# Performance work log

Hardware: AMD Instinct MI355X
Metric: run time of the kernel (lower is better)

The kernel has to match this reference:

```python
import jax, jax.numpy as jnp
import numpy as np

N_NODES = 50000
N_EDGES = 800000
IN_DIM = 128
HID_DIM = 128
OUT_DIM = 64


def setup_inputs() -> dict:
    key = jax.random.key(0)
    ks = jax.random.split(key, 6)
    x = jax.random.normal(ks[0], (N_NODES, IN_DIM), dtype=jnp.float32)
    edge_index = jax.random.randint(ks[1], (2, N_EDGES), 0, N_NODES, dtype=jnp.int64)
    # per-hop linear weights (torch Linear layout: [out, in], no bias)
    s = 1.0 / np.sqrt(IN_DIM)
    W0 = jax.random.uniform(ks[2], (HID_DIM, IN_DIM), jnp.float32, -s, s)
    W1 = jax.random.uniform(ks[3], (HID_DIM, IN_DIM), jnp.float32, -s, s)
    W2 = jax.random.uniform(ks[4], (HID_DIM, IN_DIM), jnp.float32, -s, s)
    s2 = 1.0 / np.sqrt(HID_DIM * 3)
    Wfc = jax.random.uniform(ks[5], (OUT_DIM, HID_DIM * 3), jnp.float32, -s2, s2)
    return {"x": x, "edge_index": edge_index, "W0": W0, "W1": W1, "W2": W2, "Wfc": Wfc}


def reference(x, edge_index, W0, W1, W2, Wfc):
    N = x.shape[0]
    row, col = edge_index[0], edge_index[1]  # source, target (PyG source_to_target flow)
    # symmetric degree normalization based on in-degree (degree(col, N))
    deg = jax.ops.segment_sum(jnp.ones(row.shape[0], dtype=x.dtype), col, num_segments=N)
    deg_inv_sqrt = jnp.where(deg > 0, jax.lax.rsqrt(jnp.where(deg > 0, deg, 1.0)), 0.0)
    norm = deg_inv_sqrt[row] * deg_inv_sqrt[col]  # [E]
    # NOTE: original code propagates the ORIGINAL x each iteration, so hops 1 and 2
    # both see the 1-hop propagation of x. Faithfully reproduced here.
    px = jax.ops.segment_sum(norm[:, None] * x[row], col, num_segments=N)  # [N, IN_DIM]
    # per-hop linear projections, concat over hops p=[0,1,2]
    h = jnp.concatenate([x @ W0.T, px @ W1.T, px @ W2.T], axis=1)  # [N, 3*HID_DIM]
    return h @ Wfc.T  # [N, OUT_DIM]
```

## Files before the change

### kernel.cpp

```cpp
#include <hip/hip_runtime.h>
#include <hip/hip_bf16.h>

#define N_IN  128
#define N_OUT 64
#define CFB    256
#define MAXNBC 200
#define SLACKC 5120
#define CHUNK  4096
#define PADR   136

typedef __attribute__((ext_vector_type(8))) short short8;
typedef __attribute__((ext_vector_type(4))) float floatx4;
typedef __attribute__((ext_vector_type(2))) float floatx2;

__device__ __forceinline__ unsigned pack_bf16(float a, float b) {
    __hip_bfloat16 ba = __float2bfloat16(a);
    __hip_bfloat16 bb = __float2bfloat16(b);
    unsigned short ua = *(unsigned short*)&ba;
    unsigned short ub = *(unsigned short*)&bb;
    return ((unsigned)ub << 16) | ua;
}
__device__ __forceinline__ unsigned char fp8b(float v) {
    return (unsigned char)(__builtin_amdgcn_cvt_pk_fp8_f32(v, v, 0, false) & 0xff);
}

__global__ __launch_bounds__(256) void fill_scatter(const int* __restrict__ ei,
                                                    int* __restrict__ gcur,
                                                    unsigned* __restrict__ gsorted,
                                                    const float* __restrict__ W0,
                                                    const float* __restrict__ W1,
                                                    const float* __restrict__ W2,
                                                    const float* __restrict__ Wfc,
                                                    __hip_bfloat16* __restrict__ CT,
                                                    int E, int NBC) {
    __shared__ int lcnt[MAXNBC];
    __shared__ int gbase_s[MAXNBC];
    int base = blockIdx.x * CHUNK;
    for (int i = threadIdx.x; i < NBC; i += 256) lcnt[i] = 0;
    __syncthreads();
    int myc[CHUNK / 256];
    #pragma unroll
    for (int q = 0; q < CHUNK / 256; ++q) {
        int e = base + q * 256 + threadIdx.x;
        int c = (e < E) ? ei[E + e] : -1;
        myc[q] = c;
        if (c >= 0) atomicAdd(&lcnt[c >> 8], 1);
    }
    __syncthreads();
    for (int f = threadIdx.x; f < NBC; f += 256) {
        int n = lcnt[f];
        gbase_s[f] = (n > 0) ? (f * SLACKC + atomicAdd(&gcur[f], n)) : 0;
    }
    __syncthreads();
    #pragma unroll
    for (int q = 0; q < CHUNK / 256; ++q) {
        int c = myc[q];
        if (c >= 0) {
            int e = base + q * 256 + threadIdx.x;
            unsigned r = (unsigned)ei[e];
            int p = atomicAdd(&gbase_s[c >> 8], 1);
            if (p < ((c >> 8) + 1) * SLACKC)
                gsorted[p] = ((unsigned)c << 16) | r;
        }
    }
    if (blockIdx.x < 64) {
        int t = blockIdx.x * 256 + threadIdx.x;
        int n = t >> 7;
        int i = t & 127;
        float a = 0.f;
        if (n < 64) {
            for (int k = 0; k < 128; ++k)
                a += Wfc[n * 384 + k] * W0[k * N_IN + i];
        } else {
            int o = n - 64;
            for (int k = 0; k < 128; ++k)
                a += Wfc[o * 384 + 128 + k] * W1[k * N_IN + i]
                   + Wfc[o * 384 + 256 + k] * W2[k * N_IN + i];
        }
        CT[t] = __float2bfloat16(a);
    }
}

__global__ __launch_bounds__(256) void sortgemm_kernel(
        const int* __restrict__ gcur,
        const unsigned* __restrict__ gsorted,
        unsigned short* __restrict__ srow,
        int* __restrict__ offs,
        int* __restrict__ cnt,
        float* __restrict__ dis,
        const float* __restrict__ x,
        const __hip_bfloat16* __restrict__ CT,
        float* __restrict__ out,
        unsigned char* __restrict__ z8,
        int N, int NBC) {
    __shared__ __align__(16) char smem[(64 + 128) * PADR * 2];
    int tid = threadIdx.x;

    if (blockIdx.x < NBC) {
        unsigned* ev = (unsigned*)smem;
        int* c256 = (int*)(smem + SLACKC * 4);
        int* cur  = c256 + 256;
        int* ts   = cur + 256;
        int f = blockIdx.x;
        int lo = f * SLACKC;
        int m = min(gcur[f], SLACKC);
        for (int i = tid; i < m; i += 256) ev[i] = gsorted[lo + i];
        c256[tid] = 0;
        __syncthreads();
        for (int i = tid; i < m; i += 256)
            atomicAdd(&c256[(ev[i] >> 16) & (CFB - 1)], 1);
        __syncthreads();
        int v = c256[tid];
        int xx = v;
        ts[tid] = xx;
        __syncthreads();
        for (int off = 1; off < 256; off <<= 1) {
            int t2 = (tid >= off) ? ts[tid - off] : 0;
            __syncthreads();
            xx += t2; ts[tid] = xx;
            __syncthreads();
        }
        int b = xx - v;
        cur[tid] = b;
        int node = f * CFB + tid;
        if (node < N) {
            offs[node] = lo + b;
            cnt[node] = v;
            dis[node] = v > 0 ? rsqrtf((float)v) : 0.f;
        }
        __syncthreads();
        for (int i = tid; i < m; i += 256) {
            unsigned val = ev[i];
            int cl = (val >> 16) & (CFB - 1);
            int p = atomicAdd(&cur[cl], 1);
            srow[lo + p] = (unsigned short)(val & 0xffffu);
        }
        return;
    }

    unsigned short* xs = (unsigned short*)smem;
    unsigned short* Bs = xs + 64 * PADR;
    int base = (blockIdx.x - NBC) * 64;

    {
        int row = tid >> 2;
        int colq = (tid & 3) * 32;
        int node = base + row;
        unsigned tmp[16];
        if (node < N) {
            const float4* src = (const float4*)(x + (size_t)node * N_IN + colq);
            #pragma unroll
            for (int q = 0; q < 8; ++q) {
                float4 v = src[q];
                tmp[q * 2]     = pack_bf16(v.x, v.y);
                tmp[q * 2 + 1] = pack_bf16(v.z, v.w);
            }
        } else {
            #pragma unroll
            for (int q = 0; q < 16; ++q) tmp[q] = 0u;
        }
        unsigned* dst = (unsigned*)(xs + row * PADR + colq);
        #pragma unroll
        for (int q = 0; q < 16; ++q) dst[q] = tmp[q];
    }
    {
        const unsigned* src = (const unsigned*)CT;
        for (int c = tid; c < 8192; c += 256) {
            int row = c >> 6;
            int col = (c & 63) * 2;
            *(unsigned*)(Bs + row * PADR + col) = src[c];
        }
    }
    __syncthreads();

    int wave = tid >> 6, lane = tid & 63;
    int wm = wave & 1, wn = wave >> 1;
    int quad = lane >> 4, l16 = lane & 15;

    floatx4 acc[2][4];
    #pragma unroll
    for (int mt = 0; mt < 2; ++mt)
        #pragma unroll
        for (int nt = 0; nt < 4; ++nt)
            acc[mt][nt] = (floatx4){0.f, 0.f, 0.f, 0.f};

    #pragma unroll
    for (int kc = 0; kc < 4; ++kc) {
        int kof = kc * 32 + quad * 8;
        short8 afr[2], bfr[4];
        #pragma unroll
        for (int mt = 0; mt < 2; ++mt)
            afr[mt] = *(const short8*)(xs + (wm * 32 + mt * 16 + l16) * PADR + kof);
        #pragma unroll
        for (int nt = 0; nt < 4; ++nt)
            bfr[nt] = *(const short8*)(Bs + (wn * 64 + nt * 16 + l16) * PADR + kof);
        #pragma unroll
        for (int mt = 0; mt < 2; ++mt)
            #pragma unroll
            for (int nt = 0; nt < 4; ++nt)
                acc[mt][nt] = __builtin_amdgcn_mfma_f32_16x16x32_bf16(
                    afr[mt], bfr[nt], acc[mt][nt], 0, 0, 0);
    }

    #pragma unroll
    for (int mt = 0; mt < 2; ++mt) {
        #pragma unroll
        for (int reg = 0; reg < 4; ++reg) {
            int node = base + wm * 32 + mt * 16 + quad * 4 + reg;
            if (node >= N) continue;
            if (wn == 0) {
                #pragma unroll
                for (int nt = 0; nt < 4; ++nt)
                    out[(size_t)node * N_OUT + nt * 16 + l16] = acc[mt][nt][reg];
            } else {
                #pragma unroll
                for (int nt = 0; nt < 4; ++nt)
                    z8[((size_t)node << 6) + nt * 16 + l16] = fp8b(acc[mt][nt][reg]);
            }
        }
    }
}

__global__ __launch_bounds__(256) void gather_kernel(
        const int* __restrict__ offs, const int* __restrict__ cnt,
        const unsigned short* __restrict__ srow, const unsigned char* __restrict__ z8,
        const float* __restrict__ dis, float* __restrict__ out, int N) {
    int lane = threadIdx.x & 63;
    int quarter = lane >> 4;
    int ql   = lane & 15;
    int sub  = ql >> 3;
    int jj   = ql & 7;
    int node = blockIdx.x * 16 + (threadIdx.x >> 6) * 4 + quarter;
    int start = 0, deg = 0;
    if (node < N) { start = offs[node]; deg = cnt[node]; }
    float a[8] = {0.f, 0.f, 0.f, 0.f, 0.f, 0.f, 0.f, 0.f};
    for (int k0 = 0; k0 < deg; k0 += 16) {
        int m = min(16, deg - k0);
        int idx = 0; float dv = 0.f;
        if (ql < m) {
            idx = (int)srow[start + k0 + ql];
            dv = dis[idx];
        }
        #pragma unroll
        for (int it = 0; it < 8; ++it) {
            int s0 = it * 2 + sub;
            int src0 = (lane & 48) | s0;
            int r0 = __shfl(idx, src0); float d0 = __shfl(dv, src0);
            uint2 u0 = make_uint2(0u, 0u);
            if (s0 < m) u0 = *(const uint2*)(z8 + ((size_t)r0 << 6) + jj * 8);
            floatx2 p00 = __builtin_amdgcn_cvt_pk_f32_fp8(u0.x, false);
            floatx2 p01 = __builtin_amdgcn_cvt_pk_f32_fp8(u0.x, true);
            floatx2 p02 = __builtin_amdgcn_cvt_pk_f32_fp8(u0.y, false);
            floatx2 p03 = __builtin_amdgcn_cvt_pk_f32_fp8(u0.y, true);
            a[0] += d0 * p00.x;
            a[1] += d0 * p00.y;
            a[2] += d0 * p01.x;
            a[3] += d0 * p01.y;
            a[4] += d0 * p02.x;
            a[5] += d0 * p02.y;
            a[6] += d0 * p03.x;
            a[7] += d0 * p03.y;
        }
    }
    #pragma unroll
    for (int q = 0; q < 8; ++q)
        a[q] += __shfl_xor(a[q], 8);
    if (ql < 8 && deg > 0) {
        float dn = dis[node];
        float4* op = (float4*)(out + ((size_t)node << 6) + jj * 8);
        float4 o0 = op[0], o1 = op[1];
        o0.x += dn * a[0]; o0.y += dn * a[1]; o0.z += dn * a[2]; o0.w += dn * a[3];
        o1.x += dn * a[4]; o1.y += dn * a[5]; o1.z += dn * a[6]; o1.w += dn * a[7];
        op[0] = o0; op[1] = o1;
    }
}

extern "C" void kernel_launch(void* const* d_in, const int* in_sizes, int n_in,
                              void* d_out, int out_size, void* d_ws, size_t ws_size,
                              hipStream_t stream) {
    const float* x   = (const float*)d_in[0];
    const int*   ei  = (const int*)d_in[1];
    const float* W0  = (const float*)d_in[2];
    const float* W1  = (const float*)d_in[3];
    const float* W2  = (const float*)d_in[4];
    const float* Wfc = (const float*)d_in[5];
    float* out = (float*)d_out;
    int N = in_sizes[0] / N_IN;
    int E = in_sizes[1] / 2;
    int NBC = (N + CFB - 1) / CFB;
    int GB  = (N + 63) / 64;

    __hip_bfloat16* CT = (__hip_bfloat16*)d_ws;
    int*   cnt     = (int*)((char*)d_ws + 32768);
    float* dis     = (float*)(cnt + N);
    int*   gcur    = (int*)(dis + N);
    int*   offs    = gcur + NBC;
    unsigned* gsorted = (unsigned*)(offs + N);
    unsigned short* srow = (unsigned short*)(gsorted + (size_t)NBC * SLACKC);
    size_t zoff = ((size_t)(srow + (size_t)NBC * SLACKC) - (size_t)d_ws + 63) & ~(size_t)63;
    unsigned char* z8 = (unsigned char*)d_ws + zoff;

    hipMemsetAsync(gcur, 0, (size_t)NBC * sizeof(int), stream);
    fill_scatter<<<(E + CHUNK - 1) / CHUNK, 256, 0, stream>>>(ei, gcur, gsorted,
                                                              W0, W1, W2, Wfc, CT, E, NBC);
    sortgemm_kernel<<<NBC + GB, 256, 0, stream>>>(gcur, gsorted, srow, offs, cnt, dis,
                                                  x, CT, out, z8, N, NBC);
    gather_kernel<<<(N + 15) / 16, 256, 0, stream>>>(offs, cnt, srow, z8, dis, out, N);
}
```

Measured before the change: 135.2 us.

## Fuse edge scatter into sort/GEMM kernel with spin-wait sync and prescale z

Moves the edge bucketing scatter into the front blocks of the combined sort/GEMM kernel and halves the edge chunk size. Counting blocks spin on a global atomic counter until all scatter blocks finish, so the GEMM blocks can overlap with the scatter. The weight fold and counter reset move to a small prep kernel, replacing the memset. Per-source dis scaling is folded into z by a new scale kernel that converts a bf16 z to fp8, removing the dis gather from the hot neighbor loop. In exchange it adds a bf16 round trip through memory and an extra launch. It also relies on the scatter blocks being scheduled before the spinning blocks, since otherwise the spin-wait could deadlock.

```diff
diff --git a/kernel.cpp b/kernel.cpp
--- a/kernel.cpp
+++ b/kernel.cpp
@@ -6,7 +6,7 @@
 #define CFB    256
 #define MAXNBC 200
 #define SLACKC 5120
-#define CHUNK  4096
+#define CHUNK  2048
 #define PADR   136
 
 typedef __attribute__((ext_vector_type(8))) short short8;
@@ -20,70 +20,45 @@
     unsigned short ub = *(unsigned short*)&bb;
     return ((unsigned)ub << 16) | ua;
 }
-__device__ __forceinline__ unsigned char fp8b(float v) {
-    return (unsigned char)(__builtin_amdgcn_cvt_pk_fp8_f32(v, v, 0, false) & 0xff);
-}
-
-__global__ __launch_bounds__(256) void fill_scatter(const int* __restrict__ ei,
-                                                    int* __restrict__ gcur,
-                                                    unsigned* __restrict__ gsorted,
-                                                    const float* __restrict__ W0,
-                                                    const float* __restrict__ W1,
-                                                    const float* __restrict__ W2,
-                                                    const float* __restrict__ Wfc,
-                                                    __hip_bfloat16* __restrict__ CT,
-                                                    int E, int NBC) {
-    __shared__ int lcnt[MAXNBC];
-    __shared__ int gbase_s[MAXNBC];
-    int base = blockIdx.x * CHUNK;
-    for (int i = threadIdx.x; i < NBC; i += 256) lcnt[i] = 0;
-    __syncthreads();
-    int myc[CHUNK / 256];
-    #pragma unroll
-    for (int q = 0; q < CHUNK / 256; ++q) {
-        int e = base + q * 256 + threadIdx.x;
-        int c = (e < E) ? ei[E + e] : -1;
-        myc[q] = c;
-        if (c >= 0) atomicAdd(&lcnt[c >> 8], 1);
-    }
-    __syncthreads();
-    for (int f = threadIdx.x; f < NBC; f += 256) {
-        int n = lcnt[f];
-        gbase_s[f] = (n > 0) ? (f * SLACKC + atomicAdd(&gcur[f], n)) : 0;
-    }
-    __syncthreads();
-    #pragma unroll
-    for (int q = 0; q < CHUNK / 256; ++q) {
-        int c = myc[q];
-        if (c >= 0) {
-            int e = base + q * 256 + threadIdx.x;
-            unsigned r = (unsigned)ei[e];
-            int p = atomicAdd(&gbase_s[c >> 8], 1);
-            if (p < ((c >> 8) + 1) * SLACKC)
-                gsorted[p] = ((unsigned)c << 16) | r;
-        }
-    }
-    if (blockIdx.x < 64) {
-        int t = blockIdx.x * 256 + threadIdx.x;
-        int n = t >> 7;
-        int i = t & 127;
-        float a = 0.f;
-        if (n < 64) {
-            for (int k = 0; k < 128; ++k)
-                a += Wfc[n * 384 + k] * W0[k * N_IN + i];
-        } else {
-            int o = n - 64;
-            for (int k = 0; k < 128; ++k)
-                a += Wfc[o * 384 + 128 + k] * W1[k * N_IN + i]
-                   + Wfc[o * 384 + 256 + k] * W2[k * N_IN + i];
-        }
-        CT[t] = __float2bfloat16(a);
-    }
-}
-
-__global__ __launch_bounds__(256) void sortgemm_kernel(
-        const int* __restrict__ gcur,
-        const unsigned* __restrict__ gsorted,
+__device__ __forceinline__ float bf16_to_f32(unsigned short u) {
+    unsigned v = ((unsigned)u) << 16;
+    return *(float*)&v;
+}
+
+__global__ __launch_bounds__(256) void prep_kernel(const float* __restrict__ W0,
+                                                   const float* __restrict__ W1,
+                                                   const float* __restrict__ W2,
+                                                   const float* __restrict__ Wfc,
+                                                   __hip_bfloat16* __restrict__ CT,
+                                                   int* __restrict__ gcur,
+                                                   int* __restrict__ fdone,
+                                                   int NBC) {
+    if (blockIdx.x == 0) {
+        for (int i = threadIdx.x; i < NBC; i += 256) gcur[i] = 0;
+        if (threadIdx.x == 0) *fdone = 0;
+    }
+    int t = blockIdx.x * 256 + threadIdx.x;
+    int n = t >> 7;
+    int i = t & 127;
+    float a = 0.f;
+    if (n < 64) {
+        #pragma unroll 4
+        for (int k = 0; k < 128; ++k)
+            a += Wfc[n * 384 + k] * W0[k * N_IN + i];
+    } else {
+        int o = n - 64;
+        #pragma unroll 4
+        for (int k = 0; k < 128; ++k)
+            a += Wfc[o * 384 + 128 + k] * W1[k * N_IN + i]
+               + Wfc[o * 384 + 256 + k] * W2[k * N_IN + i];
+    }
+    CT[t] = __float2bfloat16(a);
+}
+
+__global__ __launch_bounds__(256) void fused_kernel(
+        const int* __restrict__ ei,
+        int* __restrict__ gcur,
+        unsigned* __restrict__ gsorted,
         unsigned short* __restrict__ srow,
         int* __restrict__ offs,
         int* __restrict__ cnt,
@@ -91,17 +66,65 @@
         const float* __restrict__ x,
         const __hip_bfloat16* __restrict__ CT,
         float* __restrict__ out,
-        unsigned char* __restrict__ z8,
-        int N, int NBC) {
+        __hip_bfloat16* __restrict__ z16,
+        int* __restrict__ fdone,
+        int E, int N, int NBC, int NFB) {
     __shared__ __align__(16) char smem[(64 + 128) * PADR * 2];
     int tid = threadIdx.x;
-
-    if (blockIdx.x < NBC) {
+    int bid = blockIdx.x;
+
+    if (bid < NFB) {
+        int* lcnt = (int*)smem;
+        int* gbase_s = lcnt + MAXNBC;
+        int base = bid * CHUNK;
+        for (int i = tid; i < NBC; i += 256) lcnt[i] = 0;
+        __syncthreads();
+        int myc[CHUNK / 256];
+        #pragma unroll
+        for (int q = 0; q < CHUNK / 256; ++q) {
+            int e = base + q * 256 + tid;
+            int c = (e < E) ? ei[E + e] : -1;
+            myc[q] = c;
+            if (c >= 0) atomicAdd(&lcnt[c >> 8], 1);
+        }
+        __syncthreads();
+        for (int f = tid; f < NBC; f += 256) {
+            int n = lcnt[f];
+            gbase_s[f] = (n > 0) ? (f * SLACKC + atomicAdd(&gcur[f], n)) : 0;
+        }
+        __syncthreads();
+        #pragma unroll
+        for (int q = 0; q < CHUNK / 256; ++q) {
+            int c = myc[q];
+            if (c >= 0) {
+                int e = base + q * 256 + tid;
+                unsigned r = (unsigned)ei[e];
+                int p = atomicAdd(&gbase_s[c >> 8], 1);
+                if (p < ((c >> 8) + 1) * SLACKC)
+                    gsorted[p] = ((unsigned)c << 16) | r;
+            }
+        }
+        __threadfence();
+        __syncthreads();
+        if (tid == 0)
+            __hip_atomic_fetch_add(fdone, 1, __ATOMIC_RELEASE,
+                                   __HIP_MEMORY_SCOPE_AGENT);
+    }
+
+    if (bid < NBC) {
+        if (tid == 0) {
+            while (__hip_atomic_load(fdone, __ATOMIC_ACQUIRE,
+                                     __HIP_MEMORY_SCOPE_AGENT) < NFB)
+                __builtin_amdgcn_s_sleep(2);
+        }
+        __syncthreads();
+        __threadfence();
+
         unsigned* ev = (unsigned*)smem;
         int* c256 = (int*)(smem + SLACKC * 4);
         int* cur  = c256 + 256;
         int* ts   = cur + 256;
-        int f = blockIdx.x;
+        int f = bid;
         int lo = f * SLACKC;
         int m = min(gcur[f], SLACKC);
         for (int i = tid; i < m; i += 256) ev[i] = gsorted[lo + i];
@@ -140,7 +163,7 @@
 
     unsigned short* xs = (unsigned short*)smem;
     unsigned short* Bs = xs + 64 * PADR;
-    int base = (blockIdx.x - NBC) * 64;
+    int base = (bid - NBC) * 64;
 
     {
         int row = tid >> 2;
@@ -215,16 +238,40 @@
             } else {
                 #pragma unroll
                 for (int nt = 0; nt < 4; ++nt)
-                    z8[((size_t)node << 6) + nt * 16 + l16] = fp8b(acc[mt][nt][reg]);
+                    z16[((size_t)node << 6) + nt * 16 + l16] =
+                        __float2bfloat16(acc[mt][nt][reg]);
             }
         }
     }
+}
+
+__global__ __launch_bounds__(256) void scale_kernel(
+        const __hip_bfloat16* __restrict__ z16,
+        const float* __restrict__ dis,
+        unsigned char* __restrict__ z8,
+        int N) {
+    int t = blockIdx.x * 256 + threadIdx.x;
+    if (t >= N * 8) return;
+    int node = t >> 3;
+    float d = dis[node];
+    short8 v = *(const short8*)((const unsigned short*)z16 + (size_t)t * 8);
+    float f[8];
+    #pragma unroll
+    for (int j = 0; j < 8; ++j)
+        f[j] = bf16_to_f32((unsigned short)v[j]) * d;
+    unsigned lo = 0, hi = 0;
+    lo = __builtin_amdgcn_cvt_pk_fp8_f32(f[0], f[1], lo, false);
+    lo = __builtin_amdgcn_cvt_pk_fp8_f32(f[2], f[3], lo, true);
+    hi = __builtin_amdgcn_cvt_pk_fp8_f32(f[4], f[5], hi, false);
+    hi = __builtin_amdgcn_cvt_pk_fp8_f32(f[6], f[7], hi, true);
+    uint2 o; o.x = lo; o.y = hi;
+    *(uint2*)(z8 + (size_t)t * 8) = o;
 }
 
 __global__ __launch_bounds__(256) void gather_kernel(
         const int* __restrict__ offs, const int* __restrict__ cnt,
         const unsigned short* __restrict__ srow, const unsigned char* __restrict__ z8,
-        const float* __restrict__ dis, float* __restrict__ out, int N) {
+        float* __restrict__ out, int N) {
     int lane = threadIdx.x & 63;
     int quarter = lane >> 4;
     int ql   = lane & 15;
@@ -236,37 +283,35 @@
     float a[8] = {0.f, 0.f, 0.f, 0.f, 0.f, 0.f, 0.f, 0.f};
     for (int k0 = 0; k0 < deg; k0 += 16) {
         int m = min(16, deg - k0);
-        int idx = 0; float dv = 0.f;
-        if (ql < m) {
+        int idx = 0;
+        if (ql < m)
             idx = (int)srow[start + k0 + ql];
-            dv = dis[idx];
-        }
         #pragma unroll
         for (int it = 0; it < 8; ++it) {
             int s0 = it * 2 + sub;
             int src0 = (lane & 48) | s0;
-            int r0 = __shfl(idx, src0); float d0 = __shfl(dv, src0);
+            int r0 = __shfl(idx, src0);
             uint2 u0 = make_uint2(0u, 0u);
             if (s0 < m) u0 = *(const uint2*)(z8 + ((size_t)r0 << 6) + jj * 8);
             floatx2 p00 = __builtin_amdgcn_cvt_pk_f32_fp8(u0.x, false);
             floatx2 p01 = __builtin_amdgcn_cvt_pk_f32_fp8(u0.x, true);
             floatx2 p02 = __builtin_amdgcn_cvt_pk_f32_fp8(u0.y, false);
             floatx2 p03 = __builtin_amdgcn_cvt_pk_f32_fp8(u0.y, true);
-            a[0] += d0 * p00.x;
-            a[1] += d0 * p00.y;
-            a[2] += d0 * p01.x;
-            a[3] += d0 * p01.y;
-            a[4] += d0 * p02.x;
-            a[5] += d0 * p02.y;
-            a[6] += d0 * p03.x;
-            a[7] += d0 * p03.y;
+            a[0] += p00.x;
+            a[1] += p00.y;
+            a[2] += p01.x;
+            a[3] += p01.y;
+            a[4] += p02.x;
+            a[5] += p02.y;
+            a[6] += p03.x;
+            a[7] += p03.y;
         }
     }
     #pragma unroll
     for (int q = 0; q < 8; ++q)
         a[q] += __shfl_xor(a[q], 8);
     if (ql < 8 && deg > 0) {
-        float dn = dis[node];
+        float dn = rsqrtf((float)deg);
         float4* op = (float4*)(out + ((size_t)node << 6) + jj * 8);
         float4 o0 = op[0], o1 = op[1];
         o0.x += dn * a[0]; o0.y += dn * a[1]; o0.z += dn * a[2]; o0.w += dn * a[3];
@@ -289,21 +334,26 @@
     int E = in_sizes[1] / 2;
     int NBC = (N + CFB - 1) / CFB;
     int GB  = (N + 63) / 64;
+    int NFB = (E + CHUNK - 1) / CHUNK;
 
     __hip_bfloat16* CT = (__hip_bfloat16*)d_ws;
     int*   cnt     = (int*)((char*)d_ws + 32768);
     float* dis     = (float*)(cnt + N);
     int*   gcur    = (int*)(dis + N);
-    int*   offs    = gcur + NBC;
+    int*   fdone   = gcur + NBC;
+    int*   offs    = fdone + 64;
     unsigned* gsorted = (unsigned*)(offs + N);
     unsigned short* srow = (unsigned short*)(gsorted + (size_t)NBC * SLACKC);
-    size_t zoff = ((size_t)(srow + (size_t)NBC * SLACKC) - (size_t)d_ws + 63) & ~(size_t)63;
+    size_t zoff = ((size_t)((char*)(srow + (size_t)NBC * SLACKC) - (char*)d_ws) + 63)
+                  & ~(size_t)63;
     unsigned char* z8 = (unsigned char*)d_ws + zoff;
-
-    hipMemsetAsync(gcur, 0, (size_t)NBC * sizeof(int), stream);
-    fill_scatter<<<(E + CHUNK - 1) / CHUNK, 256, 0, stream>>>(ei, gcur, gsorted,
-                                                              W0, W1, W2, Wfc, CT, E, NBC);
-    sortgemm_kernel<<<NBC + GB, 256, 0, stream>>>(gcur, gsorted, srow, offs, cnt, dis,
-                                                  x, CT, out, z8, N, NBC);
-    gather_kernel<<<(N + 15) / 16, 256, 0, stream>>>(offs, cnt, srow, z8, dis, out, N);
-}
+    size_t z16off = (zoff + (size_t)N * 64 + 63) & ~(size_t)63;
+    __hip_bfloat16* z16 = (__hip_bfloat16*)((char*)d_ws + z16off);
+
+    prep_kernel<<<64, 256, 0, stream>>>(W0, W1, W2, Wfc, CT, gcur, fdone, NBC);
+    fused_kernel<<<NBC + GB, 256, 0, stream>>>(ei, gcur, gsorted, srow, offs, cnt,
+                                               dis, x, CT, out, z16, fdone,
+                                               E, N, NBC, NFB);
+    scale_kernel<<<(N * 8 + 255) / 256, 256, 0, stream>>>(z16, dis, z8, N);
+    gather_kernel<<<(N + 15) / 16, 256, 0, stream>>>(offs, cnt, srow, z8, out, N);
+}
```

Result: slower. 245.8 us (+81.8%).

## Prescale projected features by source degree norm before gather

Applied to the files above, without the earlier changes.

Moves the per-source deg^-1/2 scaling out of the edge gather loop. The GEMM now writes bf16 z, and a new scale_kernel multiplies each row by dis and quantizes it to fp8. The gather no longer loads dis[idx] per edge and computes the target norm as rsqrt(deg). This adds an extra kernel launch and a round trip through a bf16 buffer, and it also shrinks the fill_scatter CHUNK size.

```diff
diff --git a/kernel.cpp b/kernel.cpp
--- a/kernel.cpp
+++ b/kernel.cpp
@@ -6,7 +6,7 @@
 #define CFB    256
 #define MAXNBC 200
 #define SLACKC 5120
-#define CHUNK  4096
+#define CHUNK  3072
 #define PADR   136
 
 typedef __attribute__((ext_vector_type(8))) short short8;
@@ -20,8 +20,9 @@
     unsigned short ub = *(unsigned short*)&bb;
     return ((unsigned)ub << 16) | ua;
 }
-__device__ __forceinline__ unsigned char fp8b(float v) {
-    return (unsigned char)(__builtin_amdgcn_cvt_pk_fp8_f32(v, v, 0, false) & 0xff);
+__device__ __forceinline__ float bf16_to_f32(unsigned short u) {
+    unsigned v = ((unsigned)u) << 16;
+    return *(float*)&v;
 }
 
 __global__ __launch_bounds__(256) void fill_scatter(const int* __restrict__ ei,
@@ -91,7 +92,7 @@
         const float* __restrict__ x,
         const __hip_bfloat16* __restrict__ CT,
         float* __restrict__ out,
-        unsigned char* __restrict__ z8,
+        __hip_bfloat16* __restrict__ z16,
         int N, int NBC) {
     __shared__ __align__(16) char smem[(64 + 128) * PADR * 2];
     int tid = threadIdx.x;
@@ -215,16 +216,40 @@
             } else {
                 #pragma unroll
                 for (int nt = 0; nt < 4; ++nt)
-                    z8[((size_t)node << 6) + nt * 16 + l16] = fp8b(acc[mt][nt][reg]);
+                    z16[((size_t)node << 6) + nt * 16 + l16] =
+                        __float2bfloat16(acc[mt][nt][reg]);
             }
         }
     }
+}
+
+__global__ __launch_bounds__(256) void scale_kernel(
+        const __hip_bfloat16* __restrict__ z16,
+        const float* __restrict__ dis,
+        unsigned char* __restrict__ z8,
+        int N) {
+    int t = blockIdx.x * 256 + threadIdx.x;
+    if (t >= N * 8) return;
+    int node = t >> 3;
+    float d = dis[node];
+    short8 v = *(const short8*)((const unsigned short*)z16 + (size_t)t * 8);
+    float f[8];
+    #pragma unroll
+    for (int j = 0; j < 8; ++j)
+        f[j] = bf16_to_f32((unsigned short)v[j]) * d;
+    unsigned lo = 0, hi = 0;
+    lo = __builtin_amdgcn_cvt_pk_fp8_f32(f[0], f[1], lo, false);
+    lo = __builtin_amdgcn_cvt_pk_fp8_f32(f[2], f[3], lo, true);
+    hi = __builtin_amdgcn_cvt_pk_fp8_f32(f[4], f[5], hi, false);
+    hi = __builtin_amdgcn_cvt_pk_fp8_f32(f[6], f[7], hi, true);
+    uint2 o; o.x = lo; o.y = hi;
+    *(uint2*)(z8 + (size_t)t * 8) = o;
 }
 
 __global__ __launch_bounds__(256) void gather_kernel(
         const int* __restrict__ offs, const int* __restrict__ cnt,
         const unsigned short* __restrict__ srow, const unsigned char* __restrict__ z8,
-        const float* __restrict__ dis, float* __restrict__ out, int N) {
+        float* __restrict__ out, int N) {
     int lane = threadIdx.x & 63;
     int quarter = lane >> 4;
     int ql   = lane & 15;
@@ -236,37 +261,35 @@
     float a[8] = {0.f, 0.f, 0.f, 0.f, 0.f, 0.f, 0.f, 0.f};
     for (int k0 = 0; k0 < deg; k0 += 16) {
         int m = min(16, deg - k0);
-        int idx = 0; float dv = 0.f;
-        if (ql < m) {
+        int idx = 0;
+        if (ql < m)
             idx = (int)srow[start + k0 + ql];
-            dv = dis[idx];
-        }
         #pragma unroll
         for (int it = 0; it < 8; ++it) {
             int s0 = it * 2 + sub;
             int src0 = (lane & 48) | s0;
-            int r0 = __shfl(idx, src0); float d0 = __shfl(dv, src0);
+            int r0 = __shfl(idx, src0);
             uint2 u0 = make_uint2(0u, 0u);
             if (s0 < m) u0 = *(const uint2*)(z8 + ((size_t)r0 << 6) + jj * 8);
             floatx2 p00 = __builtin_amdgcn_cvt_pk_f32_fp8(u0.x, false);
             floatx2 p01 = __builtin_amdgcn_cvt_pk_f32_fp8(u0.x, true);
             floatx2 p02 = __builtin_amdgcn_cvt_pk_f32_fp8(u0.y, false);
             floatx2 p03 = __builtin_amdgcn_cvt_pk_f32_fp8(u0.y, true);
-            a[0] += d0 * p00.x;
-            a[1] += d0 * p00.y;
-            a[2] += d0 * p01.x;
-            a[3] += d0 * p01.y;
-            a[4] += d0 * p02.x;
-            a[5] += d0 * p02.y;
-            a[6] += d0 * p03.x;
-            a[7] += d0 * p03.y;
+            a[0] += p00.x;
+            a[1] += p00.y;
+            a[2] += p01.x;
+            a[3] += p01.y;
+            a[4] += p02.x;
+            a[5] += p02.y;
+            a[6] += p03.x;
+            a[7] += p03.y;
         }
     }
     #pragma unroll
     for (int q = 0; q < 8; ++q)
         a[q] += __shfl_xor(a[q], 8);
     if (ql < 8 && deg > 0) {
-        float dn = dis[node];
+        float dn = rsqrtf((float)deg);
         float4* op = (float4*)(out + ((size_t)node << 6) + jj * 8);
         float4 o0 = op[0], o1 = op[1];
         o0.x += dn * a[0]; o0.y += dn * a[1]; o0.z += dn * a[2]; o0.w += dn * a[3];
@@ -297,13 +320,17 @@
     int*   offs    = gcur + NBC;
     unsigned* gsorted = (unsigned*)(offs + N);
     unsigned short* srow = (unsigned short*)(gsorted + (size_t)NBC * SLACKC);
-    size_t zoff = ((size_t)(srow + (size_t)NBC * SLACKC) - (size_t)d_ws + 63) & ~(size_t)63;
+    size_t zoff = ((size_t)((char*)(srow + (size_t)NBC * SLACKC) - (char*)d_ws) + 63)
+                  & ~(size_t)63;
     unsigned char* z8 = (unsigned char*)d_ws + zoff;
+    size_t z16off = (zoff + (size_t)N * 64 + 63) & ~(size_t)63;
+    __hip_bfloat16* z16 = (__hip_bfloat16*)((char*)d_ws + z16off);
 
     hipMemsetAsync(gcur, 0, (size_t)NBC * sizeof(int), stream);
     fill_scatter<<<(E + CHUNK - 1) / CHUNK, 256, 0, stream>>>(ei, gcur, gsorted,
                                                               W0, W1, W2, Wfc, CT, E, NBC);
     sortgemm_kernel<<<NBC + GB, 256, 0, stream>>>(gcur, gsorted, srow, offs, cnt, dis,
-                                                  x, CT, out, z8, N, NBC);
-    gather_kernel<<<(N + 15) / 16, 256, 0, stream>>>(offs, cnt, srow, z8, dis, out, N);
-}
+                                                  x, CT, out, z16, N, NBC);
+    scale_kernel<<<(N * 8 + 255) / 256, 256, 0, stream>>>(z16, dis, z8, N);
+    gather_kernel<<<(N + 15) / 16, 256, 0, stream>>>(offs, cnt, srow, z8, out, N);
+}
```

After: 133.9 us. No clear change (-1.0%).
